# Kernel optimization log

Measured on AMD Instinct MI355X. Metric: run time of the kernel, lower is better.

The kernel has to match this reference:

```python
import jax, jax.numpy as jnp
import numpy as np
import math

B, N, D = 128, 64, 2
H, M, L = 64, 64, 2
OMEGA = 1.0


def setup_inputs() -> dict:
    key = jax.random.key(0)
    ks = jax.random.split(key, 32)
    s = 0.1  # param scale
    rn = lambda k, shp: jax.random.normal(k, shp, dtype=jnp.float32) * s
    inp = {
        "x": jax.random.normal(ks[0], (B, N, D), dtype=jnp.float32),
        "spin": jnp.zeros((B, N, 1), jnp.float32),
        "node_w1": rn(ks[1], (D + 1, H)), "node_b1": rn(ks[2], (H,)),
        "node_w2": rn(ks[3], (H, H)), "node_b2": rn(ks[4], (H,)),
        "edge_w1": rn(ks[5], (D + 2, M)), "edge_b1": rn(ks[6], (M,)),
        "edge_w2": rn(ks[7], (M, M)), "edge_b2": rn(ks[8], (M,)),
        "v2e_w1": rn(ks[9], (L, H + M, M)), "v2e_b1": rn(ks[10], (L, M)),
        "v2e_w2": rn(ks[11], (L, M, M)), "v2e_b2": rn(ks[12], (L, M)),
        "e2v_w1": rn(ks[13], (L, M, H)), "e2v_b1": rn(ks[14], (L, H)),
        "e2v_w2": rn(ks[15], (L, H, H)), "e2v_b2": rn(ks[16], (L, H)),
        "head_w1": rn(ks[17], (H, H)), "head_b1": rn(ks[18], (H,)),
        "head_w2": rn(ks[19], (H, D)), "head_b2": rn(ks[20], (D,)),
        # bf_scale_init=0.3 -> softplus-inverse
        "scale": jnp.array([math.log(math.exp(0.3) - 1.0)], jnp.float32),
    }
    return inp


def _mlp(x, w1, b1, w2, b2, act):
    return act(x @ w1 + b1) @ w2 + b2


def reference(x, spin, node_w1, node_b1, node_w2, node_b2,
              edge_w1, edge_b1, edge_w2, edge_b2,
              v2e_w1, v2e_b1, v2e_w2, v2e_b2,
              e2v_w1, e2v_b1, e2v_w2, e2v_b2,
              head_w1, head_b1, head_w2, head_b2, scale):
    gelu = lambda t: jax.nn.gelu(t, approximate=False)  # torch exact GELU
    b, n, d = x.shape
    xs = x * jnp.float32(math.sqrt(OMEGA))
    # node embedding: [B,N,H]
    hv = _mlp(jnp.concatenate([xs, spin], -1), node_w1, node_b1, node_w2, node_b2, gelu)
    # dense pairwise edge features; dr[b,i,j] = xs[b,j] - xs[b,i]
    dr = xs[:, None, :, :] - xs[:, :, None, :]            # [B,N,N,D]
    r2 = jnp.sum(dr * dr, axis=-1, keepdims=True)          # [B,N,N,1]
    rr = jnp.sqrt(r2 + 1e-12)
    he = _mlp(jnp.concatenate([dr, rr, r2], -1), edge_w1, edge_b1, edge_w2, edge_b2, gelu)  # [B,N,N,M]
    # mask excludes self-edges (i==j) from aggregation (they were never created
    # in the original edge list; their dense entries never influence off-diag values)
    mask = (1.0 - jnp.eye(n, dtype=x.dtype))[None, :, :, None]
    inv = jnp.float32(1.0 / max(n - 1, 1))
    for l in range(v2e_w1.shape[0]):
        hvb = jnp.broadcast_to(hv[:, :, None, :], (b, n, n, hv.shape[-1]))  # source node i
        he = _mlp(jnp.concatenate([hvb, he], -1), v2e_w1[l], v2e_b1[l], v2e_w2[l], v2e_b2[l], gelu)
        m = _mlp(he, e2v_w1[l], e2v_b1[l], e2v_w2[l], e2v_b2[l], gelu)      # [B,N,N,H]
        hv = hv + jnp.sum(m * mask, axis=1) * inv           # scatter-add over sources i into j
    dx = _mlp(hv, head_w1, head_b1, head_w2, head_b2, jnp.tanh) * jax.nn.softplus(scale[0])
    return dx - jnp.mean(dx, axis=1, keepdims=True)
```

## Files before the change

### kernel.cpp

```cpp
#include <hip/hip_runtime.h>
#include <math.h>


typedef unsigned short u16;
typedef unsigned int u32;
typedef _Float16 half8 __attribute__((ext_vector_type(8)));
typedef __attribute__((ext_vector_type(4))) float floatx4;

#define TS 72
#define HROW 72
#define HBLK (64 * HROW)

__device__ __forceinline__ float gelu_f(float x) {
    float s = fabsf(x) * 0.70710678118654752f;
    float q = fmaf(fmaf(fmaf(fmaf(0.078108f, s, 0.000972f), s, 0.230389f), s, 0.278393f), s, 1.0f);
    float q2 = q * q;
    float r = __builtin_amdgcn_rcpf(q2 * q2);
    float t = 0.5f * x * r;
    return x > 0.f ? x - t : t;
}

__global__ __launch_bounds__(256) void k_pre(
    const float* __restrict__ ew2, const float* __restrict__ w1he0,
    const float* __restrict__ w2_0, const float* __restrict__ u1_0,
    const float* __restrict__ w1he1, const float* __restrict__ w2_1,
    const float* __restrict__ u1_1,
    const float* __restrict__ eb2, const float* __restrict__ b2_0,
    const float* __restrict__ c1_0, const float* __restrict__ b2_1,
    const float* __restrict__ c1_1,
    const float* __restrict__ b1_0v, const float* __restrict__ b1nv,
    const float* __restrict__ u2_0, const float* __restrict__ u2_1,
    const float* __restrict__ w1n, const float* __restrict__ hw1,
    _Float16* __restrict__ WF,
    float* __restrict__ biasB, float* __restrict__ biasC, float* __restrict__ biasD,
    float* __restrict__ u2_0T, float* __restrict__ u2_1T,
    float* __restrict__ w1nT, float* __restrict__ hw1T,
    const float* __restrict__ x, const float* __restrict__ spin,
    const float* __restrict__ nw1, const float* __restrict__ nb1,
    const float* __restrict__ nw2, const float* __restrict__ nb2,
    const float* __restrict__ w1_0,
    float* __restrict__ hv, float* __restrict__ p0)
{
    int blk = blockIdx.x;
    if (blk < 64) {
        int s = blk >> 4;
        int idx = (blk & 15) * 256 + threadIdx.x;
        int k = idx >> 6, n = idx & 63;
        const float *A, *Bm;
        if (s == 0)      { A = ew2;  Bm = w1he0; }
        else if (s == 1) { A = w2_0; Bm = u1_0;  }
        else if (s == 2) { A = w2_0; Bm = w1he1; }
        else             { A = w2_1; Bm = u1_1;  }
        float acc = 0.f;
        for (int q = 0; q < 64; ++q) acc = fmaf(A[k * 64 + q], Bm[q * 64 + n], acc);
        int kc = k >> 5, qd = (k >> 3) & 3, jj = k & 7;
        WF[(((s * 2 + kc) * 64 + n) * 4 + qd) * 8 + jj] = (_Float16)acc;
    } else if (blk == 64) {
        int s = threadIdx.x >> 6, cc = threadIdx.x & 63;
        if (s > 0) {
            const float *bv, *Bm, *add; float* dst;
            if (s == 1)      { bv = b2_0; Bm = u1_0;  add = c1_0; dst = biasB; }
            else if (s == 2) { bv = b2_0; Bm = w1he1; add = b1nv; dst = biasC; }
            else             { bv = b2_1; Bm = u1_1;  add = c1_1; dst = biasD; }
            float acc = add[cc];
            for (int q = 0; q < 64; ++q) acc = fmaf(bv[q], Bm[q * 64 + cc], acc);
            dst[cc] = acc;
        }
    } else if (blk < 129) {
        int idx = (blk - 65) * 256 + threadIdx.x;
        int s = idx >> 12, r = idx & 4095, m = r >> 6, tc = r & 63;
        const float* W = s == 0 ? u2_0 : s == 1 ? u2_1 : s == 2 ? w1n : hw1;
        float* WT      = s == 0 ? u2_0T : s == 1 ? u2_1T : s == 2 ? w1nT : hw1T;
        WT[tc * 64 + m] = W[m * 64 + tc];
    } else {
        __shared__ float a[4][64];
        __shared__ float shv[4][64];
        int w = threadIdx.x >> 6, h = threadIdx.x & 63;
        int node = (blk - 129) * 4 + w;
        float2 xv = ((const float2*)x)[node];
        float sp = spin[node];
        float z = fmaf(xv.x, nw1[h], fmaf(xv.y, nw1[64 + h], fmaf(sp, nw1[128 + h], nb1[h])));
        a[w][h] = gelu_f(z);
        float acc = nb2[h];
        for (int k = 0; k < 64; ++k) acc = fmaf(a[w][k], nw2[k * 64 + h], acc);
        hv[node * 64 + h] = acc;
        shv[w][h] = acc;
        float pa = b1_0v[h];
        for (int q = 0; q < 64; ++q) pa = fmaf(eb2[q], w1he0[q * 64 + h], pa);
        for (int k = 0; k < 64; ++k) pa = fmaf(shv[w][k], w1_0[k * 64 + h], pa);
        p0[node * 64 + h] = pa;
    }
}

__device__ __forceinline__ void mfma_acc(
    const _Float16* __restrict__ tA, const _Float16* __restrict__ WF,
    int stage, int c, int quad, int nn, floatx4 acc[4])
{
    int sA = ((nn >> 2) & 3) << 3;
    #pragma unroll
    for (int kc = 0; kc < 2; ++kc) {
        half8 bf = *(const half8*)(WF + (((stage * 2 + kc) * 64 + c) * 4 + quad) * 8);
        int k0 = (kc * 32 + quad * 8) ^ sA;
        #pragma unroll
        for (int mt = 0; mt < 4; ++mt) {
            half8 af = *(const half8*)(tA + (mt * 16 + nn) * TS + k0);
            acc[mt] = __builtin_amdgcn_mfma_f32_16x16x32_f16(af, bf, acc[mt], 0, 0, 0);
        }
    }
}

__device__ __forceinline__ void init_bias(floatx4 acc[4], float bc) {
    #pragma unroll
    for (int mt = 0; mt < 4; ++mt) acc[mt] = (floatx4){bc, bc, bc, bc};
}
__device__ __forceinline__ void init_p(floatx4 acc[4], const float* __restrict__ p,
                                       int rowbase, int c, int quad) {
    #pragma unroll
    for (int mt = 0; mt < 4; ++mt)
        #pragma unroll
        for (int r = 0; r < 4; ++r)
            acc[mt][r] = p[(rowbase + mt * 16 + quad * 4 + r) * 64 + c];
}

__global__ __launch_bounds__(256, 6) void k_L0(
    const float* __restrict__ x,
    const float* __restrict__ ew1, const float* __restrict__ eb1,
    const float* __restrict__ p0,
    const float* __restrict__ biasB,
    const float* __restrict__ u2_0T, const float* __restrict__ c2_0,
    const _Float16* __restrict__ WF,
    const float* __restrict__ hv0, float* __restrict__ hv1,
    const float* __restrict__ w1nT, const float* __restrict__ biasC,
    float* __restrict__ p1,
    u16* __restrict__ he0g)
{
    __shared__ __align__(16) _Float16 tA[64 * TS];
    __shared__ float sS[64];
    __shared__ float shv[64];
    __shared__ float sred[256];
    int t = threadIdx.x, L = t & 63;
    int w = __builtin_amdgcn_readfirstlane(t >> 6);
    int nn = L & 15, quad = L >> 4;
    int c = w * 16 + nn;
    int cw = c ^ (quad << 3);
    int b = blockIdx.x >> 6, j = blockIdx.x & 63;

    float2 xi = ((const float2*)x)[b * 64 + L];
    float2 xj = ((const float2*)x)[b * 64 + j];
    float d0 = xj.x - xi.x, d1 = xj.y - xi.y;
    float r2 = fmaf(d0, d0, d1 * d1);
    float rr = sqrtf(r2 + 1e-12f);
    int swL = ((L >> 2) & 3) << 3;

    #pragma unroll
    for (int mb = 0; mb < 2; ++mb) {
        int m0 = w * 16 + mb * 8;
        half8 h8;
        #pragma unroll
        for (int kk = 0; kk < 8; ++kk) {
            int m = m0 + kk;
            float z = fmaf(d0, ew1[m], fmaf(d1, ew1[64 + m],
                      fmaf(rr, ew1[128 + m], fmaf(r2, ew1[192 + m], eb1[m]))));
            h8[kk] = (_Float16)gelu_f(z);
        }
        *(half8*)(tA + L * TS + (m0 ^ swL)) = h8;
    }
    __syncthreads();

    floatx4 acc[4];
    init_p(acc, p0, b * 64, c, quad);
    mfma_acc(tA, WF, 0, c, quad, nn, acc);
    __syncthreads();
    {
        u16* dst = he0g + (size_t)blockIdx.x * HBLK;
        #pragma unroll
        for (int mt = 0; mt < 4; ++mt)
            #pragma unroll
            for (int r = 0; r < 4; ++r) {
                int i = mt * 16 + quad * 4 + r;
                _Float16 y = (_Float16)gelu_f(acc[mt][r]);
                tA[i * TS + cw] = y;
                dst[i * HROW + cw] = __builtin_bit_cast(u16, y);
            }
    }
    __syncthreads();
    init_bias(acc, biasB[c]);
    mfma_acc(tA, WF, 1, c, quad, nn, acc);
    {
        float s = 0.f;
        #pragma unroll
        for (int mt = 0; mt < 4; ++mt)
            #pragma unroll
            for (int r = 0; r < 4; ++r) {
                int i = mt * 16 + quad * 4 + r;
                float g = gelu_f(acc[mt][r]);
                s += (i == j) ? 0.f : g;
            }
        s += __shfl_xor(s, 16);
        s += __shfl_xor(s, 32);
        if (quad == 0) sS[c] = s;
    }
    __syncthreads();
    {
        const float4* sv4 = (const float4*)(sS + w * 16);
        const float4* uv4 = (const float4*)(u2_0T + L * 64 + w * 16);
        float g = 0.f;
        #pragma unroll
        for (int m4 = 0; m4 < 4; ++m4) {
            float4 sv = sv4[m4], uv = uv4[m4];
            g = fmaf(sv.x, uv.x, fmaf(sv.y, uv.y, fmaf(sv.z, uv.z, fmaf(sv.w, uv.w, g))));
        }
        sred[w * 64 + L] = g;
    }
    __syncthreads();
    if (t < 64) {
        float g = sred[t] + sred[64 + t] + sred[128 + t] + sred[192 + t];
        int o = blockIdx.x * 64 + t;
        float hvv = hv0[o] + g * (1.0f / 63.0f) + c2_0[t];
        hv1[o] = hvv;
        shv[t] = hvv;
    }
    __syncthreads();
    {
        const float4* hv4 = (const float4*)(shv + w * 16);
        const float4* wv4 = (const float4*)(w1nT + L * 64 + w * 16);
        float pa = 0.f;
        #pragma unroll
        for (int m4 = 0; m4 < 4; ++m4) {
            float4 sv = hv4[m4], uv = wv4[m4];
            pa = fmaf(sv.x, uv.x, fmaf(sv.y, uv.y, fmaf(sv.z, uv.z, fmaf(sv.w, uv.w, pa))));
        }
        sred[w * 64 + L] = pa;
    }
    __syncthreads();
    if (t < 64)
        p1[blockIdx.x * 64 + t] = biasC[t] + sred[t] + sred[64 + t] + sred[128 + t] + sred[192 + t];
}

__global__ __launch_bounds__(256, 6) void k_L1(
    const u16* __restrict__ he0g,
    const float* __restrict__ p1,
    const float* __restrict__ biasD,
    const float* __restrict__ u2_1T, const float* __restrict__ c2_1,
    const _Float16* __restrict__ WF,
    const float* __restrict__ hv1,
    const float* __restrict__ hw1T, const float* __restrict__ hb1,
    const float* __restrict__ hw2, const float* __restrict__ hb2,
    const float* __restrict__ scale, float* __restrict__ dx)
{
    __shared__ __align__(16) _Float16 tA[64 * TS];
    __shared__ float sS[64];
    __shared__ float shv[64];
    __shared__ float sred[256];
    int t = threadIdx.x, L = t & 63;
    int w = __builtin_amdgcn_readfirstlane(t >> 6);
    int nn = L & 15, quad = L >> 4;
    int c = w * 16 + nn;
    int cw = c ^ (quad << 3);
    int b = blockIdx.x >> 6, j = blockIdx.x & 63;

    {
        const float4* src = (const float4*)(he0g + (size_t)blockIdx.x * HBLK);
        float4* dstl = (float4*)tA;
        for (int q = t; q < (HBLK * 2 / 16); q += 256)
            dstl[q] = src[q];
    }
    __syncthreads();

    floatx4 acc[4];
    init_p(acc, p1, b * 64, c, quad);
    mfma_acc(tA, WF, 2, c, quad, nn, acc);
    __syncthreads();
    #pragma unroll
    for (int mt = 0; mt < 4; ++mt)
        #pragma unroll
        for (int r = 0; r < 4; ++r)
            tA[(mt * 16 + quad * 4 + r) * TS + cw] = (_Float16)gelu_f(acc[mt][r]);
    __syncthreads();
    init_bias(acc, biasD[c]);
    mfma_acc(tA, WF, 3, c, quad, nn, acc);
    {
        float s = 0.f;
        #pragma unroll
        for (int mt = 0; mt < 4; ++mt)
            #pragma unroll
            for (int r = 0; r < 4; ++r) {
                int i = mt * 16 + quad * 4 + r;
                float g = gelu_f(acc[mt][r]);
                s += (i == j) ? 0.f : g;
            }
        s += __shfl_xor(s, 16);
        s += __shfl_xor(s, 32);
        if (quad == 0) sS[c] = s;
    }
    __syncthreads();
    {
        const float4* sv4 = (const float4*)(sS + w * 16);
        const float4* uv4 = (const float4*)(u2_1T + L * 64 + w * 16);
        float g = 0.f;
        #pragma unroll
        for (int m4 = 0; m4 < 4; ++m4) {
            float4 sv = sv4[m4], uv = uv4[m4];
            g = fmaf(sv.x, uv.x, fmaf(sv.y, uv.y, fmaf(sv.z, uv.z, fmaf(sv.w, uv.w, g))));
        }
        sred[w * 64 + L] = g;
    }
    __syncthreads();
    if (t < 64) {
        float g = sred[t] + sred[64 + t] + sred[128 + t] + sred[192 + t];
        float hv2 = hv1[blockIdx.x * 64 + t] + g * (1.0f / 63.0f) + c2_1[t];
        shv[t] = hv2;
    }
    __syncthreads();
    {
        const float4* hv4 = (const float4*)(shv + w * 16);
        const float4* wv4 = (const float4*)(hw1T + L * 64 + w * 16);
        float a = 0.f;
        #pragma unroll
        for (int m4 = 0; m4 < 4; ++m4) {
            float4 sv = hv4[m4], uv = wv4[m4];
            a = fmaf(sv.x, uv.x, fmaf(sv.y, uv.y, fmaf(sv.z, uv.z, fmaf(sv.w, uv.w, a))));
        }
        sred[w * 64 + L] = a;
    }
    __syncthreads();
    if (t < 64) {
        float a = hb1[t] + sred[t] + sred[64 + t] + sred[128 + t] + sred[192 + t];
        float t1 = tanhf(a);
        float dd0 = t1 * hw2[t * 2], dd1 = t1 * hw2[t * 2 + 1];
        #pragma unroll
        for (int off = 1; off <= 32; off <<= 1) { dd0 += __shfl_xor(dd0, off); dd1 += __shfl_xor(dd1, off); }
        if (t == 0) {
            float sp = log1pf(__expf(scale[0]));
            dx[blockIdx.x * 2 + 0] = (dd0 + hb2[0]) * sp;
            dx[blockIdx.x * 2 + 1] = (dd1 + hb2[1]) * sp;
        }
    }
}

__global__ __launch_bounds__(64) void k_mean(
    const float* __restrict__ dx, float* __restrict__ out)
{
    __shared__ float s0[64], s1[64];
    int b = blockIdx.x, j = threadIdx.x;
    float2 d = ((const float2*)dx)[b * 64 + j];
    s0[j] = d.x; s1[j] = d.y;
    __syncthreads();
    float m0 = 0.f, m1 = 0.f;
    for (int q = 0; q < 64; ++q) { m0 += s0[q]; m1 += s1[q]; }
    ((float2*)out)[b * 64 + j] = make_float2(d.x - m0 * (1.0f / 64.0f), d.y - m1 * (1.0f / 64.0f));
}

__global__ void k_beacon(float* out, float code) { out[0] = code; }

extern "C" void kernel_launch(void* const* d_in, const int* in_sizes, int n_in,
                              void* d_out, int out_size, void* d_ws, size_t ws_size,
                              hipStream_t stream)
{
    static const int exp_sizes[23] = {
        16384, 8192, 192, 64, 4096, 64,
        256, 64, 4096, 64,
        16384, 128, 8192, 128,
        8192, 128, 8192, 128,
        4096, 64, 128, 2, 1
    };
    float* hv0 = (float*)d_ws;
    float* hv1 = hv0 + 524288;
    float* p0  = hv1 + 524288;
    float* p1  = p0  + 524288;
    float* dx  = p1  + 524288;
    float* u2_0T = dx + 16384;
    float* u2_1T = u2_0T + 4096;
    float* w1nT  = u2_1T + 4096;
    float* hw1T  = w1nT + 4096;
    float* biasB = hw1T + 4096;
    float* biasC = biasB + 64;
    float* biasD = biasC + 64;
    _Float16* WF = (_Float16*)(biasD + 64);
    u16* he0g  = (u16*)(WF + 16384);
    const size_t need = (size_t)((char*)(he0g + (size_t)8192 * HBLK) - (char*)d_ws);

    int bad = -1;
    if (n_in != 23 || out_size != 16384) bad = 98;
    else if (ws_size < need) bad = 97;
    else for (int i = 0; i < 23; ++i)
        if (in_sizes[i] != exp_sizes[i]) { bad = i; break; }
    if (bad >= 0) {
        k_beacon<<<1, 1, 0, stream>>>((float*)d_out, 2e6f + bad * 1e4f);
        return;
    }

    const float* x      = (const float*)d_in[0];
    const float* spin   = (const float*)d_in[1];
    const float* nw1    = (const float*)d_in[2];
    const float* nb1    = (const float*)d_in[3];
    const float* nw2    = (const float*)d_in[4];
    const float* nb2    = (const float*)d_in[5];
    const float* ew1    = (const float*)d_in[6];
    const float* eb1    = (const float*)d_in[7];
    const float* ew2    = (const float*)d_in[8];
    const float* eb2    = (const float*)d_in[9];
    const float* v2e_w1 = (const float*)d_in[10];
    const float* v2e_b1 = (const float*)d_in[11];
    const float* v2e_w2 = (const float*)d_in[12];
    const float* v2e_b2 = (const float*)d_in[13];
    const float* e2v_w1 = (const float*)d_in[14];
    const float* e2v_b1 = (const float*)d_in[15];
    const float* e2v_w2 = (const float*)d_in[16];
    const float* e2v_b2 = (const float*)d_in[17];
    const float* hw1    = (const float*)d_in[18];
    const float* hb1    = (const float*)d_in[19];
    const float* hw2    = (const float*)d_in[20];
    const float* hb2    = (const float*)d_in[21];
    const float* scale  = (const float*)d_in[22];

    k_pre<<<2177, 256, 0, stream>>>(
        ew2, v2e_w1 + 4096, v2e_w2, e2v_w1,
        v2e_w1 + 12288, v2e_w2 + 4096, e2v_w1 + 4096,
        eb2, v2e_b2, e2v_b1, v2e_b2 + 64, e2v_b1 + 64,
        v2e_b1, v2e_b1 + 64,
        e2v_w2, e2v_w2 + 4096, v2e_w1 + 8192, hw1,
        WF, biasB, biasC, biasD,
        u2_0T, u2_1T, w1nT, hw1T,
        x, spin, nw1, nb1, nw2, nb2, v2e_w1, hv0, p0);
    k_L0<<<8192, 256, 0, stream>>>(x, ew1, eb1,
        p0, biasB, u2_0T, e2v_b2,
        WF, hv0, hv1,
        w1nT, biasC, p1,
        he0g);
    k_L1<<<8192, 256, 0, stream>>>(he0g,
        p1, biasD, u2_1T, e2v_b2 + 64,
        WF, hv1, hw1T, hb1, hw2, hb2, scale, dx);
    k_mean<<<128, 64, 0, stream>>>(dx, (float*)d_out);
}
```

Measured before the change: 234.4 us.

## Process two destination nodes per block to reuse weight fragments

Each block in k_L0 and k_L1 now handles two destination nodes j instead of one, keeping two shared-memory activation tiles and two accumulator sets. Each loaded weight fragment then feeds MFMAs for both nodes. The p-row init and edge-weight loads are also shared, and the grids are halved. The aim is to cut repeated weight loads, per-block fixed overhead and barrier count per node. The cost is double the LDS and register use, so the occupancy hint drops from 6 to 4 blocks per CU.

```diff
diff --git a/kernel.cpp b/kernel.cpp
--- a/kernel.cpp
+++ b/kernel.cpp
@@ -92,9 +92,10 @@
     }
 }
 
-__device__ __forceinline__ void mfma_acc(
-    const _Float16* __restrict__ tA, const _Float16* __restrict__ WF,
-    int stage, int c, int quad, int nn, floatx4 acc[4])
+__device__ __forceinline__ void mfma_acc2(
+    const _Float16* __restrict__ tA0, const _Float16* __restrict__ tA1,
+    const _Float16* __restrict__ WF,
+    int stage, int c, int quad, int nn, floatx4 acc0[4], floatx4 acc1[4])
 {
     int sA = ((nn >> 2) & 3) << 3;
     #pragma unroll
@@ -103,8 +104,10 @@
         int k0 = (kc * 32 + quad * 8) ^ sA;
         #pragma unroll
         for (int mt = 0; mt < 4; ++mt) {
-            half8 af = *(const half8*)(tA + (mt * 16 + nn) * TS + k0);
-            acc[mt] = __builtin_amdgcn_mfma_f32_16x16x32_f16(af, bf, acc[mt], 0, 0, 0);
+            half8 af0 = *(const half8*)(tA0 + (mt * 16 + nn) * TS + k0);
+            half8 af1 = *(const half8*)(tA1 + (mt * 16 + nn) * TS + k0);
+            acc0[mt] = __builtin_amdgcn_mfma_f32_16x16x32_f16(af0, bf, acc0[mt], 0, 0, 0);
+            acc1[mt] = __builtin_amdgcn_mfma_f32_16x16x32_f16(af1, bf, acc1[mt], 0, 0, 0);
         }
     }
 }
@@ -122,7 +125,7 @@
             acc[mt][r] = p[(rowbase + mt * 16 + quad * 4 + r) * 64 + c];
 }
 
-__global__ __launch_bounds__(256, 6) void k_L0(
+__global__ __launch_bounds__(256, 4) void k_L0(
     const float* __restrict__ x,
     const float* __restrict__ ew1, const float* __restrict__ eb1,
     const float* __restrict__ p0,
@@ -134,110 +137,144 @@
     float* __restrict__ p1,
     u16* __restrict__ he0g)
 {
-    __shared__ __align__(16) _Float16 tA[64 * TS];
-    __shared__ float sS[64];
-    __shared__ float shv[64];
-    __shared__ float sred[256];
+    __shared__ __align__(16) _Float16 tA0[64 * TS];
+    __shared__ __align__(16) _Float16 tA1[64 * TS];
+    __shared__ float sS0[64], sS1[64];
+    __shared__ float shv[2][64];
+    __shared__ float sredA[256], sredB[256];
     int t = threadIdx.x, L = t & 63;
     int w = __builtin_amdgcn_readfirstlane(t >> 6);
     int nn = L & 15, quad = L >> 4;
     int c = w * 16 + nn;
     int cw = c ^ (quad << 3);
-    int b = blockIdx.x >> 6, j = blockIdx.x & 63;
+    int b = blockIdx.x >> 5, jp = blockIdx.x & 31;
+    int j0 = jp * 2, j1 = j0 + 1;
 
     float2 xi = ((const float2*)x)[b * 64 + L];
-    float2 xj = ((const float2*)x)[b * 64 + j];
-    float d0 = xj.x - xi.x, d1 = xj.y - xi.y;
-    float r2 = fmaf(d0, d0, d1 * d1);
-    float rr = sqrtf(r2 + 1e-12f);
+    float2 xa = ((const float2*)x)[b * 64 + j0];
+    float2 xb = ((const float2*)x)[b * 64 + j1];
+    float da0 = xa.x - xi.x, da1 = xa.y - xi.y;
+    float r2a = fmaf(da0, da0, da1 * da1);
+    float rra = sqrtf(r2a + 1e-12f);
+    float db0 = xb.x - xi.x, db1 = xb.y - xi.y;
+    float r2b = fmaf(db0, db0, db1 * db1);
+    float rrb = sqrtf(r2b + 1e-12f);
     int swL = ((L >> 2) & 3) << 3;
 
     #pragma unroll
     for (int mb = 0; mb < 2; ++mb) {
         int m0 = w * 16 + mb * 8;
-        half8 h8;
+        half8 h8a, h8b;
         #pragma unroll
         for (int kk = 0; kk < 8; ++kk) {
             int m = m0 + kk;
-            float z = fmaf(d0, ew1[m], fmaf(d1, ew1[64 + m],
-                      fmaf(rr, ew1[128 + m], fmaf(r2, ew1[192 + m], eb1[m]))));
-            h8[kk] = (_Float16)gelu_f(z);
-        }
-        *(half8*)(tA + L * TS + (m0 ^ swL)) = h8;
-    }
-    __syncthreads();
-
-    floatx4 acc[4];
-    init_p(acc, p0, b * 64, c, quad);
-    mfma_acc(tA, WF, 0, c, quad, nn, acc);
-    __syncthreads();
-    {
-        u16* dst = he0g + (size_t)blockIdx.x * HBLK;
+            float e0 = ew1[m], e1 = ew1[64 + m], e2 = ew1[128 + m], e3 = ew1[192 + m], e4 = eb1[m];
+            float za = fmaf(da0, e0, fmaf(da1, e1, fmaf(rra, e2, fmaf(r2a, e3, e4))));
+            float zb = fmaf(db0, e0, fmaf(db1, e1, fmaf(rrb, e2, fmaf(r2b, e3, e4))));
+            h8a[kk] = (_Float16)gelu_f(za);
+            h8b[kk] = (_Float16)gelu_f(zb);
+        }
+        *(half8*)(tA0 + L * TS + (m0 ^ swL)) = h8a;
+        *(half8*)(tA1 + L * TS + (m0 ^ swL)) = h8b;
+    }
+    __syncthreads();
+
+    floatx4 acc0[4], acc1[4];
+    init_p(acc0, p0, b * 64, c, quad);
+    #pragma unroll
+    for (int mt = 0; mt < 4; ++mt) acc1[mt] = acc0[mt];
+    mfma_acc2(tA0, tA1, WF, 0, c, quad, nn, acc0, acc1);
+    __syncthreads();
+    {
+        u16* dst0 = he0g + (size_t)(b * 64 + j0) * HBLK;
+        u16* dst1 = he0g + (size_t)(b * 64 + j1) * HBLK;
         #pragma unroll
         for (int mt = 0; mt < 4; ++mt)
             #pragma unroll
             for (int r = 0; r < 4; ++r) {
                 int i = mt * 16 + quad * 4 + r;
-                _Float16 y = (_Float16)gelu_f(acc[mt][r]);
-                tA[i * TS + cw] = y;
-                dst[i * HROW + cw] = __builtin_bit_cast(u16, y);
+                _Float16 ya = (_Float16)gelu_f(acc0[mt][r]);
+                _Float16 yb = (_Float16)gelu_f(acc1[mt][r]);
+                tA0[i * TS + cw] = ya;
+                tA1[i * TS + cw] = yb;
+                dst0[i * HROW + cw] = __builtin_bit_cast(u16, ya);
+                dst1[i * HROW + cw] = __builtin_bit_cast(u16, yb);
             }
     }
     __syncthreads();
-    init_bias(acc, biasB[c]);
-    mfma_acc(tA, WF, 1, c, quad, nn, acc);
-    {
-        float s = 0.f;
+    {
+        float bb = biasB[c];
+        init_bias(acc0, bb);
+        init_bias(acc1, bb);
+    }
+    mfma_acc2(tA0, tA1, WF, 1, c, quad, nn, acc0, acc1);
+    {
+        float s0 = 0.f, s1 = 0.f;
         #pragma unroll
         for (int mt = 0; mt < 4; ++mt)
             #pragma unroll
             for (int r = 0; r < 4; ++r) {
                 int i = mt * 16 + quad * 4 + r;
-                float g = gelu_f(acc[mt][r]);
-                s += (i == j) ? 0.f : g;
+                float ga = gelu_f(acc0[mt][r]);
+                float gb = gelu_f(acc1[mt][r]);
+                s0 += (i == j0) ? 0.f : ga;
+                s1 += (i == j1) ? 0.f : gb;
             }
-        s += __shfl_xor(s, 16);
-        s += __shfl_xor(s, 32);
-        if (quad == 0) sS[c] = s;
-    }
-    __syncthreads();
-    {
-        const float4* sv4 = (const float4*)(sS + w * 16);
+        s0 += __shfl_xor(s0, 16); s0 += __shfl_xor(s0, 32);
+        s1 += __shfl_xor(s1, 16); s1 += __shfl_xor(s1, 32);
+        if (quad == 0) { sS0[c] = s0; sS1[c] = s1; }
+    }
+    __syncthreads();
+    {
+        const float4* sv0 = (const float4*)(sS0 + w * 16);
+        const float4* sv1 = (const float4*)(sS1 + w * 16);
         const float4* uv4 = (const float4*)(u2_0T + L * 64 + w * 16);
-        float g = 0.f;
+        float g0 = 0.f, g1 = 0.f;
         #pragma unroll
         for (int m4 = 0; m4 < 4; ++m4) {
-            float4 sv = sv4[m4], uv = uv4[m4];
-            g = fmaf(sv.x, uv.x, fmaf(sv.y, uv.y, fmaf(sv.z, uv.z, fmaf(sv.w, uv.w, g))));
-        }
-        sred[w * 64 + L] = g;
-    }
-    __syncthreads();
-    if (t < 64) {
-        float g = sred[t] + sred[64 + t] + sred[128 + t] + sred[192 + t];
-        int o = blockIdx.x * 64 + t;
-        float hvv = hv0[o] + g * (1.0f / 63.0f) + c2_0[t];
+            float4 uv = uv4[m4], a0 = sv0[m4], a1 = sv1[m4];
+            g0 = fmaf(a0.x, uv.x, fmaf(a0.y, uv.y, fmaf(a0.z, uv.z, fmaf(a0.w, uv.w, g0))));
+            g1 = fmaf(a1.x, uv.x, fmaf(a1.y, uv.y, fmaf(a1.z, uv.z, fmaf(a1.w, uv.w, g1))));
+        }
+        sredA[w * 64 + L] = g0;
+        sredB[w * 64 + L] = g1;
+    }
+    __syncthreads();
+    if (t < 128) {
+        int h = t & 63, sj = t >> 6;
+        const float* sr = sj ? sredB : sredA;
+        float g = sr[h] + sr[64 + h] + sr[128 + h] + sr[192 + h];
+        int jj = sj ? j1 : j0;
+        int o = (b * 64 + jj) * 64 + h;
+        float hvv = hv0[o] + g * (1.0f / 63.0f) + c2_0[h];
         hv1[o] = hvv;
-        shv[t] = hvv;
-    }
-    __syncthreads();
-    {
-        const float4* hv4 = (const float4*)(shv + w * 16);
+        shv[sj][h] = hvv;
+    }
+    __syncthreads();
+    {
+        const float4* h0 = (const float4*)(shv[0] + w * 16);
+        const float4* h1 = (const float4*)(shv[1] + w * 16);
         const float4* wv4 = (const float4*)(w1nT + L * 64 + w * 16);
-        float pa = 0.f;
+        float pa = 0.f, pb = 0.f;
         #pragma unroll
         for (int m4 = 0; m4 < 4; ++m4) {
-            float4 sv = hv4[m4], uv = wv4[m4];
-            pa = fmaf(sv.x, uv.x, fmaf(sv.y, uv.y, fmaf(sv.z, uv.z, fmaf(sv.w, uv.w, pa))));
-        }
-        sred[w * 64 + L] = pa;
-    }
-    __syncthreads();
-    if (t < 64)
-        p1[blockIdx.x * 64 + t] = biasC[t] + sred[t] + sred[64 + t] + sred[128 + t] + sred[192 + t];
-}
-
-__global__ __launch_bounds__(256, 6) void k_L1(
+            float4 wv = wv4[m4], a0 = h0[m4], a1 = h1[m4];
+            pa = fmaf(a0.x, wv.x, fmaf(a0.y, wv.y, fmaf(a0.z, wv.z, fmaf(a0.w, wv.w, pa))));
+            pb = fmaf(a1.x, wv.x, fmaf(a1.y, wv.y, fmaf(a1.z, wv.z, fmaf(a1.w, wv.w, pb))));
+        }
+        sredA[w * 64 + L] = pa;
+        sredB[w * 64 + L] = pb;
+    }
+    __syncthreads();
+    if (t < 128) {
+        int h = t & 63, sj = t >> 6;
+        const float* sr = sj ? sredB : sredA;
+        int jj = sj ? j1 : j0;
+        p1[(b * 64 + jj) * 64 + h] = biasC[h] + sr[h] + sr[64 + h] + sr[128 + h] + sr[192 + h];
+    }
+}
+
+__global__ __launch_bounds__(256, 4) void k_L1(
     const u16* __restrict__ he0g,
     const float* __restrict__ p1,
     const float* __restrict__ biasD,
@@ -248,92 +285,118 @@
     const float* __restrict__ hw2, const float* __restrict__ hb2,
     const float* __restrict__ scale, float* __restrict__ dx)
 {
-    __shared__ __align__(16) _Float16 tA[64 * TS];
-    __shared__ float sS[64];
-    __shared__ float shv[64];
-    __shared__ float sred[256];
+    __shared__ __align__(16) _Float16 tA0[64 * TS];
+    __shared__ __align__(16) _Float16 tA1[64 * TS];
+    __shared__ float sS0[64], sS1[64];
+    __shared__ float shv[2][64];
+    __shared__ float sredA[256], sredB[256];
     int t = threadIdx.x, L = t & 63;
     int w = __builtin_amdgcn_readfirstlane(t >> 6);
     int nn = L & 15, quad = L >> 4;
     int c = w * 16 + nn;
     int cw = c ^ (quad << 3);
-    int b = blockIdx.x >> 6, j = blockIdx.x & 63;
-
-    {
-        const float4* src = (const float4*)(he0g + (size_t)blockIdx.x * HBLK);
-        float4* dstl = (float4*)tA;
-        for (int q = t; q < (HBLK * 2 / 16); q += 256)
-            dstl[q] = src[q];
-    }
-    __syncthreads();
-
-    floatx4 acc[4];
-    init_p(acc, p1, b * 64, c, quad);
-    mfma_acc(tA, WF, 2, c, quad, nn, acc);
+    int b = blockIdx.x >> 5, jp = blockIdx.x & 31;
+    int j0 = jp * 2, j1 = j0 + 1;
+
+    {
+        const float4* s0 = (const float4*)(he0g + (size_t)(b * 64 + j0) * HBLK);
+        const float4* s1 = (const float4*)(he0g + (size_t)(b * 64 + j1) * HBLK);
+        float4* d0 = (float4*)tA0;
+        float4* d1 = (float4*)tA1;
+        for (int q = t; q < (HBLK * 2 / 16); q += 256) { d0[q] = s0[q]; d1[q] = s1[q]; }
+    }
+    __syncthreads();
+
+    floatx4 acc0[4], acc1[4];
+    init_p(acc0, p1, b * 64, c, quad);
+    #pragma unroll
+    for (int mt = 0; mt < 4; ++mt) acc1[mt] = acc0[mt];
+    mfma_acc2(tA0, tA1, WF, 2, c, quad, nn, acc0, acc1);
     __syncthreads();
     #pragma unroll
     for (int mt = 0; mt < 4; ++mt)
         #pragma unroll
-        for (int r = 0; r < 4; ++r)
-            tA[(mt * 16 + quad * 4 + r) * TS + cw] = (_Float16)gelu_f(acc[mt][r]);
-    __syncthreads();
-    init_bias(acc, biasD[c]);
-    mfma_acc(tA, WF, 3, c, quad, nn, acc);
-    {
-        float s = 0.f;
+        for (int r = 0; r < 4; ++r) {
+            int i = mt * 16 + quad * 4 + r;
+            tA0[i * TS + cw] = (_Float16)gelu_f(acc0[mt][r]);
+            tA1[i * TS + cw] = (_Float16)gelu_f(acc1[mt][r]);
+        }
+    __syncthreads();
+    {
+        float bd = biasD[c];
+        init_bias(acc0, bd);
+        init_bias(acc1, bd);
+    }
+    mfma_acc2(tA0, tA1, WF, 3, c, quad, nn, acc0, acc1);
+    {
+        float s0 = 0.f, s1 = 0.f;
         #pragma unroll
         for (int mt = 0; mt < 4; ++mt)
             #pragma unroll
             for (int r = 0; r < 4; ++r) {
                 int i = mt * 16 + quad * 4 + r;
-                float g = gelu_f(acc[mt][r]);
-                s += (i == j) ? 0.f : g;
+                float ga = gelu_f(acc0[mt][r]);
+                float gb = gelu_f(acc1[mt][r]);
+                s0 += (i == j0) ? 0.f : ga;
+                s1 += (i == j1) ? 0.f : gb;
             }
-        s += __shfl_xor(s, 16);
-        s += __shfl_xor(s, 32);
-        if (quad == 0) sS[c] = s;
-    }
-    __syncthreads();
-    {
-        const float4* sv4 = (const float4*)(sS + w * 16);
+        s0 += __shfl_xor(s0, 16); s0 += __shfl_xor(s0, 32);
+        s1 += __shfl_xor(s1, 16); s1 += __shfl_xor(s1, 32);
+        if (quad == 0) { sS0[c] = s0; sS1[c] = s1; }
+    }
+    __syncthreads();
+    {
+        const float4* sv0 = (const float4*)(sS0 + w * 16);
+        const float4* sv1 = (const float4*)(sS1 + w * 16);
         const float4* uv4 = (const float4*)(u2_1T + L * 64 + w * 16);
-        float g = 0.f;
+        float g0 = 0.f, g1 = 0.f;
         #pragma unroll
         for (int m4 = 0; m4 < 4; ++m4) {
-            float4 sv = sv4[m4], uv = uv4[m4];
-            g = fmaf(sv.x, uv.x, fmaf(sv.y, uv.y, fmaf(sv.z, uv.z, fmaf(sv.w, uv.w, g))));
-        }
-        sred[w * 64 + L] = g;
-    }
-    __syncthreads();
-    if (t < 64) {
-        float g = sred[t] + sred[64 + t] + sred[128 + t] + sred[192 + t];
-        float hv2 = hv1[blockIdx.x * 64 + t] + g * (1.0f / 63.0f) + c2_1[t];
-        shv[t] = hv2;
-    }
-    __syncthreads();
-    {
-        const float4* hv4 = (const float4*)(shv + w * 16);
+            float4 uv = uv4[m4], a0 = sv0[m4], a1 = sv1[m4];
+            g0 = fmaf(a0.x, uv.x, fmaf(a0.y, uv.y, fmaf(a0.z, uv.z, fmaf(a0.w, uv.w, g0))));
+            g1 = fmaf(a1.x, uv.x, fmaf(a1.y, uv.y, fmaf(a1.z, uv.z, fmaf(a1.w, uv.w, g1))));
+        }
+        sredA[w * 64 + L] = g0;
+        sredB[w * 64 + L] = g1;
+    }
+    __syncthreads();
+    if (t < 128) {
+        int h = t & 63, sj = t >> 6;
+        const float* sr = sj ? sredB : sredA;
+        float g = sr[h] + sr[64 + h] + sr[128 + h] + sr[192 + h];
+        int jj = sj ? j1 : j0;
+        float hv2 = hv1[(b * 64 + jj) * 64 + h] + g * (1.0f / 63.0f) + c2_1[h];
+        shv[sj][h] = hv2;
+    }
+    __syncthreads();
+    {
+        const float4* h0 = (const float4*)(shv[0] + w * 16);
+        const float4* h1 = (const float4*)(shv[1] + w * 16);
         const float4* wv4 = (const float4*)(hw1T + L * 64 + w * 16);
-        float a = 0.f;
+        float a0 = 0.f, a1 = 0.f;
         #pragma unroll
         for (int m4 = 0; m4 < 4; ++m4) {
-            float4 sv = hv4[m4], uv = wv4[m4];
-            a = fmaf(sv.x, uv.x, fmaf(sv.y, uv.y, fmaf(sv.z, uv.z, fmaf(sv.w, uv.w, a))));
-        }
-        sred[w * 64 + L] = a;
-    }
-    __syncthreads();
-    if (t < 64) {
-        float a = hb1[t] + sred[t] + sred[64 + t] + sred[128 + t] + sred[192 + t];
+            float4 wv = wv4[m4], v0 = h0[m4], v1 = h1[m4];
+            a0 = fmaf(v0.x, wv.x, fmaf(v0.y, wv.y, fmaf(v0.z, wv.z, fmaf(v0.w, wv.w, a0))));
+            a1 = fmaf(v1.x, wv.x, fmaf(v1.y, wv.y, fmaf(v1.z, wv.z, fmaf(v1.w, wv.w, a1))));
+        }
+        sredA[w * 64 + L] = a0;
+        sredB[w * 64 + L] = a1;
+    }
+    __syncthreads();
+    if (t < 128) {
+        int h = t & 63, sj = t >> 6;
+        const float* sr = sj ? sredB : sredA;
+        float a = hb1[h] + sr[h] + sr[64 + h] + sr[128 + h] + sr[192 + h];
         float t1 = tanhf(a);
-        float dd0 = t1 * hw2[t * 2], dd1 = t1 * hw2[t * 2 + 1];
+        float dd0 = t1 * hw2[h * 2], dd1 = t1 * hw2[h * 2 + 1];
         #pragma unroll
         for (int off = 1; off <= 32; off <<= 1) { dd0 += __shfl_xor(dd0, off); dd1 += __shfl_xor(dd1, off); }
-        if (t == 0) {
+        if (h == 0) {
+            int jj = sj ? j1 : j0;
             float sp = log1pf(__expf(scale[0]));
-            dx[blockIdx.x * 2 + 0] = (dd0 + hb2[0]) * sp;
-            dx[blockIdx.x * 2 + 1] = (dd1 + hb2[1]) * sp;
+            dx[(b * 64 + jj) * 2 + 0] = (dd0 + hb2[0]) * sp;
+            dx[(b * 64 + jj) * 2 + 1] = (dd1 + hb2[1]) * sp;
         }
     }
 }
@@ -423,12 +486,12 @@
         WF, biasB, biasC, biasD,
         u2_0T, u2_1T, w1nT, hw1T,
         x, spin, nw1, nb1, nw2, nb2, v2e_w1, hv0, p0);
-    k_L0<<<8192, 256, 0, stream>>>(x, ew1, eb1,
+    k_L0<<<4096, 256, 0, stream>>>(x, ew1, eb1,
         p0, biasB, u2_0T, e2v_b2,
         WF, hv0, hv1,
         w1nT, biasC, p1,
         he0g);
-    k_L1<<<8192, 256, 0, stream>>>(he0g,
+    k_L1<<<4096, 256, 0, stream>>>(he0g,
         p1, biasD, u2_1T, e2v_b2 + 64,
         WF, hv1, hw1T, hb1, hw2, hb2, scale, dx);
     k_mean<<<128, 64, 0, stream>>>(dx, (float*)d_out);
```

Result: faster. 212.1 us (-9.5%).
